# Kernel tuning notes

Hardware: AMD Instinct MI355X
Metric: run time of the kernel (lower is better)

Reference implementation:

```python
import jax, jax.numpy as jnp
import numpy as np

B, L, DIN = 2048, 70, 15
HID, NF, K = 16, 4, 40          # hidden_units//2, n_features, kernel_size
C = DIN + 1 + NF                # 20 signature input channels (original + time + conv features)
Z0 = 64
SIG_CH = C + C * C + C ** 3     # 8420, depth-3 signature channels


def setup_inputs() -> dict:
    key = jax.random.key(0)
    ks = jax.random.split(key, 8)
    return {
        "observed_data": jax.random.normal(ks[0], (B, L, DIN), jnp.float32),
        "observed_tp": jnp.linspace(0.0, 1.0, L, dtype=jnp.float32),
        "conv1_w": jax.random.normal(ks[1], (HID, DIN, K), jnp.float32) / np.float32(np.sqrt(DIN * K)),
        "conv1_b": jnp.zeros((HID,), jnp.float32),
        "conv2_w": jax.random.normal(ks[2], (HID, HID), jnp.float32) / np.float32(np.sqrt(HID)),
        "conv2_b": jnp.zeros((HID,), jnp.float32),
        "conv3_w": jax.random.normal(ks[3], (NF, HID), jnp.float32) / np.float32(np.sqrt(HID)),
        "conv3_b": jnp.zeros((NF,), jnp.float32),
        "w_out": jax.random.normal(ks[4], (2 * Z0, SIG_CH), jnp.float32) * np.float32(np.sqrt(2.0 / (SIG_CH + 2 * Z0))),
        "b_out": jnp.zeros((2 * Z0,), jnp.float32),
    }


def _augment(x, w1, b1, w2, b2, w3, b3):
    # x: (B, L, DIN).  signatory.Augment: conv(K) -> relu -> conv1x1 -> relu -> conv1x1,
    # then concat [truncated original, time channel, conv features] along channels.
    xc = jnp.transpose(x, (0, 2, 1))                                   # (B, DIN, L)
    h = jax.lax.conv_general_dilated(xc, w1, (1,), 'VALID')            # (B, HID, Lp)
    h = h + b1[None, :, None]
    h = jnp.einsum('oc,bcl->bol', w2, jax.nn.relu(h)) + b2[None, :, None]
    h = jnp.einsum('oc,bcl->bol', w3, jax.nn.relu(h)) + b3[None, :, None]
    conv_out = jnp.transpose(h, (0, 2, 1))                             # (B, Lp, NF)
    Lp = conv_out.shape[1]
    orig = x[:, K - 1:, :]                                             # (B, Lp, DIN)
    t = jnp.linspace(0.0, 1.0, Lp, dtype=x.dtype)
    time = jnp.broadcast_to(t[None, :, None], (x.shape[0], Lp, 1))
    return jnp.concatenate([orig, time, conv_out], axis=2)             # (B, Lp, C)


def _signature_depth3(path):
    # Truncated (depth 3) path signature with basepoint=True, via Chen's identity:
    # S <- S \otimes exp(dx) over increments, zero basepoint prepended.
    incs = jnp.diff(path, axis=1, prepend=jnp.zeros_like(path[:, :1]))  # (B, Lp, C)
    incs = jnp.transpose(incs, (1, 0, 2))                               # (Lp, B, C)
    Bn, Cn = path.shape[0], path.shape[2]
    s1 = jnp.zeros((Bn, Cn), path.dtype)
    s2 = jnp.zeros((Bn, Cn, Cn), path.dtype)
    s3 = jnp.zeros((Bn, Cn, Cn, Cn), path.dtype)

    def step(carry, d):
        s1, s2, s3 = carry
        e2 = 0.5 * d[:, :, None] * d[:, None, :]                        # d\otimes d / 2
        e3 = (e2[:, :, :, None] * d[:, None, None, :]) / 3.0            # d^{\otimes 3} / 6
        n3 = (s3
              + s2[:, :, :, None] * d[:, None, None, :]
              + s1[:, :, None, None] * e2[:, None, :, :]
              + e3)
        n2 = s2 + s1[:, :, None] * d[:, None, :] + e2
        n1 = s1 + d
        return (n1, n2, n3), None

    (s1, s2, s3), _ = jax.lax.scan(step, (s1, s2, s3), incs)
    return jnp.concatenate([s1, s2.reshape(Bn, -1), s3.reshape(Bn, -1)], axis=1)


def reference(observed_data, observed_tp, conv1_w, conv1_b, conv2_w, conv2_b,
              conv3_w, conv3_b, w_out, b_out):
    # encode_obs_time=False -> observed_tp unused
    path = _augment(observed_data, conv1_w, conv1_b, conv2_w, conv2_b, conv3_w, conv3_b)
    sig = _signature_depth3(path)                                       # (B, SIG_CH)
    z = sig @ w_out.T + b_out                                           # (B, 2*Z0)
    mean_z0 = z[:, :Z0][None]                                           # (1, B, Z0)
    std_z0 = jax.nn.softplus(z[:, Z0:][None])                           # (1, B, Z0)
    return mean_z0, std_z0
```

## Files before the change

### kernel.cpp

```cpp
#include <hip/hip_runtime.h>
#include <math.h>

#define B_TOT 2048
#define D_INC 15
#define KW    40
#define CCH   20
#define LP    31
#define SIGCH 8420
#define SIGP  8448
#define NOUT  128
#define KSPLIT 11
#define KLEN  768

typedef _Float16 f16;
typedef _Float16 f16x8 __attribute__((ext_vector_type(8)));
typedef _Float16 f16x4 __attribute__((ext_vector_type(4)));
typedef _Float16 f16x2 __attribute__((ext_vector_type(2)));
typedef float    f32x4 __attribute__((ext_vector_type(4)));

__global__ __launch_bounds__(256) void k_prep(const float* __restrict__ w1,
                                              f16* __restrict__ wA)
{
    const int ln = threadIdx.x & 63;
    const int wv = threadIdx.x >> 6;
    const int h  = ln & 15;
    const int q4 = ln >> 4;
    for (int gi = 0; gi < 5; ++gi) {
        int g = wv * 5 + gi;
        f16x8 v;
#pragma unroll
        for (int j = 0; j < 8; ++j) {
            int kq = q4 * 8 + j;
            int kk = 2 * g + (kq >> 4);
            int c  = kq & 15;
            v[j] = (c < D_INC) ? (f16)w1[h * 600 + c * 40 + kk] : (f16)0.f;
        }
        *(f16x8*)(wA + g * 512 + ln * 8) = v;
    }
}

__global__ __launch_bounds__(64, 4) void k_augsig(
    const float* __restrict__ x,  const f16* __restrict__ wA, const float* __restrict__ b1,
    const float* __restrict__ w2, const float* __restrict__ b2,
    const float* __restrict__ w3, const float* __restrict__ b3,
    const float* __restrict__ w_out, f16* __restrict__ wh, f16* __restrict__ sig)
{
    if (blockIdx.x >= 2048) {
        int t0 = (blockIdx.x - 2048) * 64 + threadIdx.x;
        for (int chunk = t0; chunk < 128 * 1056; chunk += 8192) {
            int o  = chunk / 1056;
            int cw = chunk - o * 1056;
            int c0 = cw * 8;
            f16x8 v;
            if (c0 + 8 <= SIGCH) {
                const float* src = w_out + (size_t)o * SIGCH + c0;
                float4 a = *(const float4*)src;
                float4 b = *(const float4*)(src + 4);
                v = (f16x8){(f16)a.x,(f16)a.y,(f16)a.z,(f16)a.w,
                            (f16)b.x,(f16)b.y,(f16)b.z,(f16)b.w};
            } else {
#pragma unroll
                for (int e = 0; e < 8; ++e) {
                    int c = c0 + e;
                    v[e] = (c < SIGCH) ? (f16)w_out[(size_t)o * SIGCH + c] : (f16)0.f;
                }
            }
            *(f16x8*)(wh + (size_t)o * SIGP + c0) = v;
        }
        return;
    }

    __shared__ float pool[3364];
    float* xs    = pool;
    f16*   xp16  = (f16*)(pool + 1068);
    float* h1s   = (float*)xp16;
    float* pprev = pool + 2352;
    float* wsmall= pool + 3008;
    float* w2s = wsmall;        float* b2s = wsmall + 256;
    float* w3s = wsmall + 272;  float* b3s = wsmall + 336;
    float* b1s = wsmall + 340;

    const int lane = threadIdx.x;
    const int b    = blockIdx.x;
    const int n16  = lane & 15;
    const int q4   = lane >> 4;

    for (int i = lane; i < 1050; i += 64) xs[i] = x[(size_t)b * 1050 + i];
    for (int i = lane; i < 256; i += 64) w2s[i] = w2[i];
    w3s[lane] = w3[lane];
    if (lane < 16) b2s[lane] = b2[lane];
    if (lane < 4)  b3s[lane] = b3[lane];
    if (lane < 16) b1s[lane] = b1[lane];

    f16x8 wa[20];
#pragma unroll
    for (int g = 0; g < 20; ++g) wa[g] = *(const f16x8*)(wA + g * 512 + lane * 8);
    __syncthreads();

    for (int pos = lane; pos < 70; pos += 64) {
        const float* src = xs + pos * 15;
        f16* dst = xp16 + pos * 16;
#pragma unroll
        for (int c = 0; c < 15; ++c) dst[c] = (f16)src[c];
        dst[15] = (f16)0.f;
    }
    __syncthreads();

    f32x4 cacc[2];
#pragma unroll
    for (int tile = 0; tile < 2; ++tile) {
        const int pos0 = tile * 15;
        f32x4 acc = {0.f, 0.f, 0.f, 0.f};
#pragma unroll
        for (int g = 0; g < 20; ++g) {
            const f16x8 bf = *(const f16x8*)&xp16[
                (pos0 + n16 + 2 * g + (q4 >> 1)) * 16 + (q4 & 1) * 8];
            acc = __builtin_amdgcn_mfma_f32_16x16x32_f16(wa[g], bf, acc, 0, 0, 0);
        }
        cacc[tile] = acc;
    }
    __syncthreads();

#pragma unroll
    for (int tile = 0; tile < 2; ++tile) {
        int pos = tile * 15 + n16;
#pragma unroll
        for (int r = 0; r < 4; ++r) {
            int h = q4 * 4 + r;
            h1s[pos * 17 + h] = fmaxf(cacc[tile][r] + b1s[h], 0.f);
        }
    }
    __syncthreads();

    if (lane < 31) {
        const int pos = lane;
        float hr[16];
#pragma unroll
        for (int c2 = 0; c2 < 16; ++c2) hr[c2] = h1s[pos * 17 + c2];
        float h2[16];
#pragma unroll
        for (int o = 0; o < 16; ++o) {
            float s = b2s[o];
#pragma unroll
            for (int c2 = 0; c2 < 16; ++c2) s += w2s[o * 16 + c2] * hr[c2];
            h2[o] = fmaxf(s, 0.f);
        }
        float h3[4];
#pragma unroll
        for (int f = 0; f < 4; ++f) {
            float s = b3s[f];
#pragma unroll
            for (int c2 = 0; c2 < 16; ++c2) s += w3s[f * 16 + c2] * h2[c2];
            h3[f] = s;
        }
        float* pr = pprev + 20 + pos * 20;
#pragma unroll
        for (int d = 0; d < D_INC; ++d) pr[d] = xs[(pos + 39) * 15 + d];
        pr[15] = (float)pos * (1.0f / 30.0f);
#pragma unroll
        for (int f = 0; f < 4; ++f) pr[16 + f] = h3[f];
    } else {
        int z = lane - 31;
        if (z < 20) pprev[z] = 0.f;
    }
    __syncthreads();

    float* pp   = pprev;
    f16*   scr  = (f16*)pool;
    f16*   dtr  = scr;
    f16*   atr  = scr + 800;
    f16*   etr  = scr + 1600;
    f16*   Vb   = scr + 2400;

    for (int e = lane; e < 620; e += 64) {
        int c = e / 31, t = e - c * 31;
        float p0 = pp[t * 20 + c];
        float d  = pp[(t + 1) * 20 + c] - p0;
        dtr[c * 40 + t] = (f16)d;
        atr[c * 40 + t] = (f16)(p0 + 0.5f * d);
        etr[c * 40 + t] = (f16)(0.5f * p0 + d * (1.0f / 6.0f));
    }
    if (lane < 20) {
        dtr[lane * 40 + 31] = (f16)0.f;
        atr[lane * 40 + 31] = (f16)0.f;
        etr[lane * 40 + 31] = (f16)0.f;
    }
    __syncthreads();

    if (lane < 20) {
        f16* vr = Vb + lane * 72;
        float s = 0.f;
        for (int t = 30; t >= 0; --t) {
            float dv = (float)dtr[lane * 40 + t];
            vr[t]      = (f16)s;
            vr[32 + t] = (f16)dv;
            s += dv;
        }
        vr[31] = (f16)0.f;
        vr[63] = (f16)0.f;
    } else if (lane == 20) {
        f16* vr = Vb + 20 * 72;
        for (int k = 0; k < 64; ++k) vr[k] = (k < 31) ? (f16)1.f : (f16)0.f;
    }
    for (int e = lane; e < 11 * 32; e += 64) {
        int row = 21 + (e >> 5);
        int kk  = (e & 31) * 2;
        *(f16x2*)(Vb + row * 72 + kk) = (f16x2){(f16)0.f, (f16)0.f};
    }
    __syncthreads();

    f16x8 bf[2][2];
#pragma unroll
    for (int kc = 0; kc < 2; ++kc)
#pragma unroll
        for (int nt = 0; nt < 2; ++nt)
            bf[kc][nt] = *(const f16x8*)(Vb + (nt * 16 + n16) * 72 + kc * 32 + q4 * 8);

    f16* sg = sig + (size_t)b * SIGP;

    for (int mt = 0; mt < 25; ++mt) {
        const int p = mt * 16 + n16;
        const int i = p / 20, j = p - i * 20;
        f16x8 av = *(const f16x8*)(atr + i * 40 + q4 * 8);
        f16x8 ev = *(const f16x8*)(etr + i * 40 + q4 * 8);
        f16x8 dv = *(const f16x8*)(dtr + j * 40 + q4 * 8);
        f16x8 uf = av * dv;
        f16x8 ef = ev * dv;

        f32x4 a0 = {0.f,0.f,0.f,0.f}, a1 = {0.f,0.f,0.f,0.f};
        a0 = __builtin_amdgcn_mfma_f32_16x16x32_f16(bf[0][0], uf, a0, 0, 0, 0);
        a0 = __builtin_amdgcn_mfma_f32_16x16x32_f16(bf[1][0], ef, a0, 0, 0, 0);
        a1 = __builtin_amdgcn_mfma_f32_16x16x32_f16(bf[0][1], uf, a1, 0, 0, 0);
        a1 = __builtin_amdgcn_mfma_f32_16x16x32_f16(bf[1][1], ef, a1, 0, 0, 0);

        f16x4 s0 = {(f16)a0[0], (f16)a0[1], (f16)a0[2], (f16)a0[3]};
        *(f16x4*)(sg + 420 + p * 20 + q4 * 4) = s0;
        if (q4 == 0) {
            f16x4 s1v = {(f16)a1[0], (f16)a1[1], (f16)a1[2], (f16)a1[3]};
            *(f16x4*)(sg + 420 + p * 20 + 16) = s1v;
        } else if (q4 == 1) {
            sg[20 + p] = (f16)a1[0];
        }
    }

    if (lane < 20) sg[lane] = (f16)pp[620 + lane];
    if (lane < 28) sg[SIGCH + lane] = (f16)0.f;
}

__global__ __launch_bounds__(256) void k_gemm(const f16* __restrict__ sigh,
                                              const f16* __restrict__ wh,
                                              float* __restrict__ z_part)
{
    __shared__ f16 As[2048];
    __shared__ f16 Bs[8192];
    const int tid = threadIdx.x;
    const int l   = tid & 63;
    const int wv  = tid >> 6;
    const int mt  = blockIdx.x / KSPLIT;
    const int s   = blockIdx.x - mt * KSPLIT;
    const int m0  = mt * 32;
    const int kb  = s * KLEN;

    const f32x4 z4 = {0.f, 0.f, 0.f, 0.f};
    f32x4 acc[2][2];
    acc[0][0] = z4; acc[0][1] = z4; acc[1][0] = z4; acc[1][1] = z4;

    const size_t gA = (size_t)(m0 + (tid & 31)) * SIGP + kb + (tid >> 5) * 8;
    size_t gB[4];
#pragma unroll
    for (int r = 0; r < 4; ++r) {
        int slot = r * 256 + tid;
        gB[r] = (size_t)(slot & 127) * SIGP + kb + (slot >> 7) * 8;
    }

    f16x8 aR = *(const f16x8*)(sigh + gA);
    f16x8 bR[4];
#pragma unroll
    for (int r = 0; r < 4; ++r) bR[r] = *(const f16x8*)(wh + gB[r]);

    const int kg   = l >> 4;
    const int mrow = l & 15;

    for (int ch = 0; ch < 12; ++ch) {
        *(f16x8*)&As[tid * 8] = aR;
#pragma unroll
        for (int r = 0; r < 4; ++r) *(f16x8*)&Bs[(r * 256 + tid) * 8] = bR[r];
        __syncthreads();

        if (ch < 11) {
            int koff = (ch + 1) * 64;
            aR = *(const f16x8*)(sigh + gA + koff);
#pragma unroll
            for (int r = 0; r < 4; ++r) bR[r] = *(const f16x8*)(wh + gB[r] + koff);
        }

#pragma unroll
        for (int kc = 0; kc < 2; ++kc) {
            f16x8 aF[2], bF[2];
#pragma unroll
            for (int m2 = 0; m2 < 2; ++m2)
                aF[m2] = *(const f16x8*)&As[((kc * 4 + kg) * 32 + m2 * 16 + mrow) * 8];
#pragma unroll
            for (int n2 = 0; n2 < 2; ++n2)
                bF[n2] = *(const f16x8*)&Bs[((kc * 4 + kg) * 128 + wv * 32 + n2 * 16 + mrow) * 8];
#pragma unroll
            for (int m2 = 0; m2 < 2; ++m2)
#pragma unroll
                for (int n2 = 0; n2 < 2; ++n2)
                    acc[m2][n2] = __builtin_amdgcn_mfma_f32_16x16x32_f16(aF[m2], bF[n2], acc[m2][n2], 0, 0, 0);
        }
        __syncthreads();
    }

#pragma unroll
    for (int m2 = 0; m2 < 2; ++m2) {
#pragma unroll
        for (int n2 = 0; n2 < 2; ++n2) {
            int n = wv * 32 + n2 * 16 + (l & 15);
#pragma unroll
            for (int r = 0; r < 4; ++r) {
                int m = m0 + m2 * 16 + (l >> 4) * 4 + r;
                z_part[((size_t)s * B_TOT + m) * NOUT + n] = acc[m2][n2][r];
            }
        }
    }
}

__global__ __launch_bounds__(256) void k_final(const float* __restrict__ z_part,
                                               const float* __restrict__ b_out,
                                               float* __restrict__ out)
{
    int idx = blockIdx.x * 256 + threadIdx.x;
    int b = idx >> 7;
    int o = idx & 127;
    float z = b_out[o];
#pragma unroll
    for (int s = 0; s < KSPLIT; ++s) z += z_part[((size_t)s * B_TOT + b) * NOUT + o];
    if (o < 64) {
        out[(size_t)b * 64 + o] = z;
    } else {
        float sp = fmaxf(z, 0.f) + log1pf(expf(-fabsf(z)));
        out[131072 + (size_t)b * 64 + (o - 64)] = sp;
    }
}

extern "C" void kernel_launch(void* const* d_in, const int* in_sizes, int n_in,
                              void* d_out, int out_size, void* d_ws, size_t ws_size,
                              hipStream_t stream)
{
    const float* x     = (const float*)d_in[0];
    const float* w1    = (const float*)d_in[2];
    const float* b1    = (const float*)d_in[3];
    const float* w2    = (const float*)d_in[4];
    const float* b2    = (const float*)d_in[5];
    const float* w3    = (const float*)d_in[6];
    const float* b3    = (const float*)d_in[7];
    const float* w_out = (const float*)d_in[8];
    const float* b_out = (const float*)d_in[9];
    float* out = (float*)d_out;

    float* ws    = (float*)d_ws;
    f16*   sigh  = (f16*)ws;
    f16*   wh    = (f16*)(ws + 8650752);
    f16*   wA    = (f16*)(ws + 9191424);
    float* zpart = ws + 9196544;

    hipLaunchKernelGGL(k_prep,   dim3(1),    dim3(256), 0, stream, w1, wA);
    hipLaunchKernelGGL(k_augsig, dim3(2176), dim3(64),  0, stream,
                       x, wA, b1, w2, b2, w3, b3, w_out, wh, sigh);
    hipLaunchKernelGGL(k_gemm,   dim3(704),  dim3(256), 0, stream, sigh, wh, zpart);
    hipLaunchKernelGGL(k_final,  dim3(1024), dim3(256), 0, stream, zpart, b_out, out);
}
```

Before: 135.8 us.

## Split augment+signature block across two wavefronts and parallelize suffix sums

Each batch element's k_augsig block now runs two wavefronts instead of one. The two conv tiles go one per wave, the 1x1 conv layers are split across 124 threads with an extra shared buffer and barrier, and the 25 signature MFMA tiles are divided 13/12 between the waves. The serial per-channel reverse cumulative sum is replaced by a parallel formula, total minus prefix, taken from the path values. This cuts per-block serial latency at the cost of more threads, more shared memory and an extra barrier, which may reduce block occupancy.

```diff
diff --git a/kernel.cpp b/kernel.cpp
--- a/kernel.cpp
+++ b/kernel.cpp
@@ -39,14 +39,14 @@
     }
 }
 
-__global__ __launch_bounds__(64, 4) void k_augsig(
+__global__ __launch_bounds__(128, 4) void k_augsig(
     const float* __restrict__ x,  const f16* __restrict__ wA, const float* __restrict__ b1,
     const float* __restrict__ w2, const float* __restrict__ b2,
     const float* __restrict__ w3, const float* __restrict__ b3,
     const float* __restrict__ w_out, f16* __restrict__ wh, f16* __restrict__ sig)
 {
     if (blockIdx.x >= 2048) {
-        int t0 = (blockIdx.x - 2048) * 64 + threadIdx.x;
+        int t0 = (blockIdx.x - 2048) * 128 + threadIdx.x;
         for (int chunk = t0; chunk < 128 * 1056; chunk += 8192) {
             int o  = chunk / 1056;
             int cw = chunk - o * 1056;
@@ -70,34 +70,37 @@
         return;
     }
 
-    __shared__ float pool[3364];
+    __shared__ float pool[3891];
     float* xs    = pool;
     f16*   xp16  = (f16*)(pool + 1068);
     float* h1s   = (float*)xp16;
     float* pprev = pool + 2352;
     float* wsmall= pool + 3008;
+    float* h2s   = pool + 3364;
     float* w2s = wsmall;        float* b2s = wsmall + 256;
     float* w3s = wsmall + 272;  float* b3s = wsmall + 336;
     float* b1s = wsmall + 340;
 
-    const int lane = threadIdx.x;
+    const int tid  = threadIdx.x;
+    const int lane = tid & 63;
+    const int wv   = tid >> 6;
     const int b    = blockIdx.x;
     const int n16  = lane & 15;
     const int q4   = lane >> 4;
 
-    for (int i = lane; i < 1050; i += 64) xs[i] = x[(size_t)b * 1050 + i];
-    for (int i = lane; i < 256; i += 64) w2s[i] = w2[i];
-    w3s[lane] = w3[lane];
-    if (lane < 16) b2s[lane] = b2[lane];
-    if (lane < 4)  b3s[lane] = b3[lane];
-    if (lane < 16) b1s[lane] = b1[lane];
+    for (int i = tid; i < 1050; i += 128) xs[i] = x[(size_t)b * 1050 + i];
+    for (int i = tid; i < 256; i += 128) w2s[i] = w2[i];
+    if (tid < 64) w3s[tid] = w3[tid];
+    if (tid < 16) b2s[tid] = b2[tid];
+    if (tid < 4)  b3s[tid] = b3[tid];
+    if (tid < 16) b1s[tid] = b1[tid];
 
     f16x8 wa[20];
 #pragma unroll
     for (int g = 0; g < 20; ++g) wa[g] = *(const f16x8*)(wA + g * 512 + lane * 8);
     __syncthreads();
 
-    for (int pos = lane; pos < 70; pos += 64) {
+    for (int pos = tid; pos < 70; pos += 128) {
         const float* src = xs + pos * 15;
         f16* dst = xp16 + pos * 16;
 #pragma unroll
@@ -106,63 +109,59 @@
     }
     __syncthreads();
 
-    f32x4 cacc[2];
-#pragma unroll
-    for (int tile = 0; tile < 2; ++tile) {
-        const int pos0 = tile * 15;
-        f32x4 acc = {0.f, 0.f, 0.f, 0.f};
+    f32x4 cacc = {0.f, 0.f, 0.f, 0.f};
+    {
+        const int pos0 = wv * 15;
 #pragma unroll
         for (int g = 0; g < 20; ++g) {
-            const f16x8 bf = *(const f16x8*)&xp16[
+            const f16x8 bfv = *(const f16x8*)&xp16[
                 (pos0 + n16 + 2 * g + (q4 >> 1)) * 16 + (q4 & 1) * 8];
-            acc = __builtin_amdgcn_mfma_f32_16x16x32_f16(wa[g], bf, acc, 0, 0, 0);
-        }
-        cacc[tile] = acc;
-    }
-    __syncthreads();
-
-#pragma unroll
-    for (int tile = 0; tile < 2; ++tile) {
-        int pos = tile * 15 + n16;
+            cacc = __builtin_amdgcn_mfma_f32_16x16x32_f16(wa[g], bfv, cacc, 0, 0, 0);
+        }
+    }
+    __syncthreads();
+
+    {
+        int pos = wv * 15 + n16;
 #pragma unroll
         for (int r = 0; r < 4; ++r) {
             int h = q4 * 4 + r;
-            h1s[pos * 17 + h] = fmaxf(cacc[tile][r] + b1s[h], 0.f);
-        }
-    }
-    __syncthreads();
-
-    if (lane < 31) {
-        const int pos = lane;
+            h1s[pos * 17 + h] = fmaxf(cacc[r] + b1s[h], 0.f);
+        }
+    }
+    __syncthreads();
+
+    if (tid < 124) {
+        const int og  = tid / 31;
+        const int pos = tid - og * 31;
         float hr[16];
 #pragma unroll
         for (int c2 = 0; c2 < 16; ++c2) hr[c2] = h1s[pos * 17 + c2];
-        float h2[16];
-#pragma unroll
-        for (int o = 0; o < 16; ++o) {
+#pragma unroll
+        for (int oo = 0; oo < 4; ++oo) {
+            int o = og * 4 + oo;
             float s = b2s[o];
 #pragma unroll
             for (int c2 = 0; c2 < 16; ++c2) s += w2s[o * 16 + c2] * hr[c2];
-            h2[o] = fmaxf(s, 0.f);
-        }
-        float h3[4];
-#pragma unroll
-        for (int f = 0; f < 4; ++f) {
-            float s = b3s[f];
-#pragma unroll
-            for (int c2 = 0; c2 < 16; ++c2) s += w3s[f * 16 + c2] * h2[c2];
-            h3[f] = s;
-        }
-        float* pr = pprev + 20 + pos * 20;
-#pragma unroll
-        for (int d = 0; d < D_INC; ++d) pr[d] = xs[(pos + 39) * 15 + d];
-        pr[15] = (float)pos * (1.0f / 30.0f);
-#pragma unroll
-        for (int f = 0; f < 4; ++f) pr[16 + f] = h3[f];
-    } else {
-        int z = lane - 31;
-        if (z < 20) pprev[z] = 0.f;
-    }
+            h2s[pos * 17 + o] = fmaxf(s, 0.f);
+        }
+    }
+    __syncthreads();
+
+    if (tid < 124) {
+        const int f   = tid / 31;
+        const int pos = tid - f * 31;
+        float s = b3s[f];
+#pragma unroll
+        for (int c2 = 0; c2 < 16; ++c2) s += w3s[f * 16 + c2] * h2s[pos * 17 + c2];
+        pprev[20 + pos * 20 + 16 + f] = s;
+    }
+    for (int e = tid; e < 465; e += 128) {
+        int pos = e / 15, d = e - pos * 15;
+        pprev[20 + pos * 20 + d] = xs[(pos + 39) * 15 + d];
+    }
+    if (tid < 31) pprev[20 + tid * 20 + 15] = (float)tid * (1.0f / 30.0f);
+    if (tid < 20) pprev[tid] = 0.f;
     __syncthreads();
 
     float* pp   = pprev;
@@ -172,7 +171,7 @@
     f16*   etr  = scr + 1600;
     f16*   Vb   = scr + 2400;
 
-    for (int e = lane; e < 620; e += 64) {
+    for (int e = tid; e < 620; e += 128) {
         int c = e / 31, t = e - c * 31;
         float p0 = pp[t * 20 + c];
         float d  = pp[(t + 1) * 20 + c] - p0;
@@ -180,45 +179,44 @@
         atr[c * 40 + t] = (f16)(p0 + 0.5f * d);
         etr[c * 40 + t] = (f16)(0.5f * p0 + d * (1.0f / 6.0f));
     }
-    if (lane < 20) {
-        dtr[lane * 40 + 31] = (f16)0.f;
-        atr[lane * 40 + 31] = (f16)0.f;
-        etr[lane * 40 + 31] = (f16)0.f;
-    }
-    __syncthreads();
-
-    if (lane < 20) {
-        f16* vr = Vb + lane * 72;
-        float s = 0.f;
-        for (int t = 30; t >= 0; --t) {
-            float dv = (float)dtr[lane * 40 + t];
-            vr[t]      = (f16)s;
-            vr[32 + t] = (f16)dv;
-            s += dv;
-        }
-        vr[31] = (f16)0.f;
-        vr[63] = (f16)0.f;
-    } else if (lane == 20) {
-        f16* vr = Vb + 20 * 72;
-        for (int k = 0; k < 64; ++k) vr[k] = (k < 31) ? (f16)1.f : (f16)0.f;
-    }
-    for (int e = lane; e < 11 * 32; e += 64) {
-        int row = 21 + (e >> 5);
-        int kk  = (e & 31) * 2;
+    if (tid < 20) {
+        dtr[tid * 40 + 31] = (f16)0.f;
+        atr[tid * 40 + 31] = (f16)0.f;
+        etr[tid * 40 + 31] = (f16)0.f;
+    }
+
+    for (int e = tid; e < 640; e += 128) {
+        int n = e >> 5, t = e & 31;
+        f16* vr = Vb + n * 72;
+        if (t < 31) {
+            float pt = pp[(t + 1) * 20 + n];
+            vr[t]      = (f16)(pp[620 + n] - pt);
+            vr[32 + t] = (f16)(pt - pp[t * 20 + n]);
+        } else {
+            vr[31] = (f16)0.f;
+            vr[63] = (f16)0.f;
+        }
+    }
+    if (tid < 64) Vb[20 * 72 + tid] = (tid < 31) ? (f16)1.f : (f16)0.f;
+    for (int u = tid; u < 352; u += 128) {
+        int row = 21 + (u >> 5);
+        int kk  = (u & 31) * 2;
         *(f16x2*)(Vb + row * 72 + kk) = (f16x2){(f16)0.f, (f16)0.f};
     }
     __syncthreads();
 
-    f16x8 bf[2][2];
+    f16x8 bfr[2][2];
 #pragma unroll
     for (int kc = 0; kc < 2; ++kc)
 #pragma unroll
         for (int nt = 0; nt < 2; ++nt)
-            bf[kc][nt] = *(const f16x8*)(Vb + (nt * 16 + n16) * 72 + kc * 32 + q4 * 8);
+            bfr[kc][nt] = *(const f16x8*)(Vb + (nt * 16 + n16) * 72 + kc * 32 + q4 * 8);
 
     f16* sg = sig + (size_t)b * SIGP;
 
-    for (int mt = 0; mt < 25; ++mt) {
+    const int mtB = wv ? 13 : 0;
+    const int mtE = wv ? 25 : 13;
+    for (int mt = mtB; mt < mtE; ++mt) {
         const int p = mt * 16 + n16;
         const int i = p / 20, j = p - i * 20;
         f16x8 av = *(const f16x8*)(atr + i * 40 + q4 * 8);
@@ -228,10 +226,10 @@
         f16x8 ef = ev * dv;
 
         f32x4 a0 = {0.f,0.f,0.f,0.f}, a1 = {0.f,0.f,0.f,0.f};
-        a0 = __builtin_amdgcn_mfma_f32_16x16x32_f16(bf[0][0], uf, a0, 0, 0, 0);
-        a0 = __builtin_amdgcn_mfma_f32_16x16x32_f16(bf[1][0], ef, a0, 0, 0, 0);
-        a1 = __builtin_amdgcn_mfma_f32_16x16x32_f16(bf[0][1], uf, a1, 0, 0, 0);
-        a1 = __builtin_amdgcn_mfma_f32_16x16x32_f16(bf[1][1], ef, a1, 0, 0, 0);
+        a0 = __builtin_amdgcn_mfma_f32_16x16x32_f16(bfr[0][0], uf, a0, 0, 0, 0);
+        a0 = __builtin_amdgcn_mfma_f32_16x16x32_f16(bfr[1][0], ef, a0, 0, 0, 0);
+        a1 = __builtin_amdgcn_mfma_f32_16x16x32_f16(bfr[0][1], uf, a1, 0, 0, 0);
+        a1 = __builtin_amdgcn_mfma_f32_16x16x32_f16(bfr[1][1], ef, a1, 0, 0, 0);
 
         f16x4 s0 = {(f16)a0[0], (f16)a0[1], (f16)a0[2], (f16)a0[3]};
         *(f16x4*)(sg + 420 + p * 20 + q4 * 4) = s0;
@@ -243,8 +241,8 @@
         }
     }
 
-    if (lane < 20) sg[lane] = (f16)pp[620 + lane];
-    if (lane < 28) sg[SIGCH + lane] = (f16)0.f;
+    if (tid < 20) sg[tid] = (f16)pp[620 + tid];
+    if (tid < 28) sg[SIGCH + tid] = (f16)0.f;
 }
 
 __global__ __launch_bounds__(256) void k_gemm(const f16* __restrict__ sigh,
@@ -366,7 +364,7 @@
     float* zpart = ws + 9196544;
 
     hipLaunchKernelGGL(k_prep,   dim3(1),    dim3(256), 0, stream, w1, wA);
-    hipLaunchKernelGGL(k_augsig, dim3(2176), dim3(64),  0, stream,
+    hipLaunchKernelGGL(k_augsig, dim3(2112), dim3(128), 0, stream,
                        x, wA, b1, w2, b2, w3, b3, w_out, wh, sigh);
     hipLaunchKernelGGL(k_gemm,   dim3(704),  dim3(256), 0, stream, sigh, wh, zpart);
     hipLaunchKernelGGL(k_final,  dim3(1024), dim3(256), 0, stream, zpart, b_out, out);
```

Result: no change. 138.3 us (+1.8%).
